# Performance work log

Hardware: AMD Instinct MI355X
Metric: run time of the kernel (lower is better)

## Reference

```python
import jax, jax.numpy as jnp
import numpy as np
from jax.ops import segment_sum

N_NODES = 50000
N_EDGES = 800000
D_IN, D_HID, D_OUT = 128, 128, 64


def setup_inputs() -> dict:
    key = jax.random.key(0)
    ks = jax.random.split(key, 7)
    return {
        "src": jax.random.randint(ks[0], (N_EDGES,), 0, N_NODES, dtype=jnp.int32),
        "dst": jax.random.randint(ks[1], (N_EDGES,), 0, N_NODES, dtype=jnp.int32),
        "x": jax.random.normal(ks[2], (N_NODES, D_IN), dtype=jnp.float32),
        "W1": jax.random.normal(ks[3], (D_IN, D_HID), dtype=jnp.float32) * (1.0 / np.sqrt(D_IN)),
        "b1": jnp.zeros((D_HID,), dtype=jnp.float32),
        "W2": jax.random.normal(ks[4], (D_HID, D_OUT), dtype=jnp.float32) * (1.0 / np.sqrt(D_HID)),
        "b2": jnp.zeros((D_OUT,), dtype=jnp.float32),
    }


def _gcn_layer(src, dst, x, W, b, inv_sqrt_out, inv_sqrt_in):
    # DGL GraphConv, norm='both': h = D_in^{-1/2} A D_out^{-1/2} (x W) + b
    h = (x * inv_sqrt_out[:, None]) @ W          # transform first (in >= out)
    msg = h[src]                                  # gather source messages [E, d]
    agg = segment_sum(msg, dst, num_segments=x.shape[0])
    return agg * inv_sqrt_in[:, None] + b


def reference(src, dst, x, W1, b1, W2, b2):
    n = x.shape[0]
    ones = jnp.ones((src.shape[0],), dtype=x.dtype)
    deg_out = jnp.clip(segment_sum(ones, src, num_segments=n), 1.0)
    deg_in = jnp.clip(segment_sum(ones, dst, num_segments=n), 1.0)
    inv_sqrt_out = jax.lax.rsqrt(deg_out)
    inv_sqrt_in = jax.lax.rsqrt(deg_in)
    h = _gcn_layer(src, dst, x, W1, b1, inv_sqrt_out, inv_sqrt_in)
    h = jax.nn.relu(h)
    h = _gcn_layer(src, dst, h, W2, b2, inv_sqrt_out, inv_sqrt_in)
    return h
```

## Files before the change

### kernel.cpp

```cpp
#include <hip/hip_runtime.h>
#include <hip/hip_fp16.h>

#define D_IN  128
#define D_HID 128
#define D_OUT 64
#define NBMAX 512
#define CHUNK 2048
#define FCACHE 3072

typedef __attribute__((ext_vector_type(8))) short bf16x8;
typedef __attribute__((ext_vector_type(4))) float f32x4;

__device__ __forceinline__ unsigned short f2bf_rne(float f) {
    unsigned int u = __float_as_uint(f);
    return (unsigned short)((u + 0x7FFFu + ((u >> 16) & 1u)) >> 16);
}

__global__ void k_zero(int* __restrict__ cntD, int* __restrict__ cntS, int NB) {
    const int t = threadIdx.x;
    if (t < NB) { cntD[t] = 0; cntS[t] = 0; }
}

__launch_bounds__(256)
__global__ void k_bucket(const int* __restrict__ src, const int* __restrict__ dst,
                         int E, int NB, int cap,
                         int* __restrict__ cntD, int* __restrict__ cntS,
                         unsigned int* __restrict__ storeD, unsigned char* __restrict__ storeS) {
    __shared__ int lcD[NBMAX], lcS[NBMAX];
    __shared__ int lbD[NBMAX], lbS[NBMAX];
    const int t = threadIdx.x;
    const int e0 = blockIdx.x * CHUNK;
    const int e1 = min(e0 + CHUNK, E);

    for (int i = t; i < NB; i += 256) { lcD[i] = 0; lcS[i] = 0; }
    __syncthreads();
    for (int i = e0 + t; i < e1; i += 256) {
        atomicAdd(&lcD[dst[i] >> 7], 1);
        atomicAdd(&lcS[src[i] >> 7], 1);
    }
    __syncthreads();
    for (int i = t; i < NB; i += 256) {
        lbD[i] = lcD[i] ? atomicAdd(&cntD[i], lcD[i]) : 0;
        lbS[i] = lcS[i] ? atomicAdd(&cntS[i], lcS[i]) : 0;
        lcD[i] = 0; lcS[i] = 0;
    }
    __syncthreads();
    for (int i = e0 + t; i < e1; i += 256) {
        const int s = src[i], d = dst[i];
        const int bd = d >> 7;
        const int pd = lbD[bd] + atomicAdd(&lcD[bd], 1);
        storeD[(long long)bd * cap + pd] = (unsigned int)s | ((unsigned int)(d & 127) << 16);
        const int bs = s >> 7;
        const int ps = lbS[bs] + atomicAdd(&lcS[bs], 1);
        storeS[(long long)bs * cap + ps] = (unsigned char)(s & 127);
    }
}

__launch_bounds__(256)
__global__ void k_fin(const unsigned int* __restrict__ storeD, const unsigned char* __restrict__ storeS,
                      const int* __restrict__ cntD, const int* __restrict__ cntS,
                      int cap, int N, int NB, int E,
                      int* __restrict__ rowptr, float* __restrict__ inv_in,
                      float* __restrict__ inv_out, unsigned short* __restrict__ csr_src) {
    __shared__ int fh[128];
    __shared__ int sc[128];
    __shared__ int cur[128];
    __shared__ int red[256];
    __shared__ unsigned int ecache[FCACHE];
    const int b = blockIdx.x, t = threadIdx.x;
    const long long sb = (long long)b * cap;

    int partial = 0;
    for (int i = t; i < b; i += 256) partial += cntD[i];
    red[t] = partial;
    __syncthreads();
    for (int off = 128; off > 0; off >>= 1) {
        if (t < off) red[t] += red[t + off];
        __syncthreads();
    }
    const int base = red[0];

    const int cnt = cntD[b];
    const bool cached = (cnt <= FCACHE);
    if (cached) {
        for (int i = t; i < cnt; i += 256) ecache[i] = storeD[sb + i];
    }

    if (t < 128) fh[t] = 0;
    __syncthreads();
    for (int i = t; i < cnt; i += 256) {
        const unsigned int e = cached ? ecache[i] : storeD[sb + i];
        atomicAdd(&fh[e >> 16], 1);
    }
    __syncthreads();
    if (t < 128) sc[t] = fh[t];
    __syncthreads();
    int inc = (t < 128) ? sc[t] : 0;
    for (int off = 1; off < 128; off <<= 1) {
        int o = (t >= off && t < 128) ? sc[t - off] : 0;
        __syncthreads();
        if (t < 128) { inc += o; sc[t] = inc; }
        __syncthreads();
    }
    if (t < 128) {
        const int excl = inc - fh[t];
        cur[t] = excl;
        const int node = (b << 7) + t;
        if (node < N) {
            rowptr[node] = base + excl;
            inv_in[node] = rsqrtf((float)max(fh[t], 1));
        }
    }
    if (b == NB - 1 && t == 128) rowptr[N] = E;
    __syncthreads();
    for (int i = t; i < cnt; i += 256) {
        const unsigned int e = cached ? ecache[i] : storeD[sb + i];
        const int pos = atomicAdd(&cur[e >> 16], 1);
        csr_src[base + pos] = (unsigned short)(e & 0xFFFFu);
    }

    __syncthreads();
    if (t < 128) fh[t] = 0;
    __syncthreads();
    const int cnts = cntS[b];
    for (int i = t; i < cnts; i += 256) atomicAdd(&fh[storeS[sb + i]], 1);
    __syncthreads();
    if (t < 128) {
        const int node = (b << 7) + t;
        if (node < N) inv_out[node] = rsqrtf((float)max(fh[t], 1));
    }
}

template<int LDN, typename TA>
__launch_bounds__(256)
__global__ void k_gemm_mfma(const TA* __restrict__ X, const float* __restrict__ W,
                            const float* __restrict__ scale, __half* __restrict__ Y, int N) {
    __shared__ short Ah[32][136], Al[32][136];
    __shared__ short Bh[64][136], Bl[64][136];

    const int t = threadIdx.x;
    const int row0 = blockIdx.x * 32;
    const int col0 = blockIdx.y * 64;

    if constexpr (sizeof(TA) == 4) {
#pragma unroll
        for (int p = 0; p < 4; ++p) {
            const int idx = p * 256 + t;
            const int r   = idx >> 5;
            const int c4  = (idx & 31) << 2;
            const int gr  = row0 + r;
            float4 v = make_float4(0.f, 0.f, 0.f, 0.f);
            if (gr < N) {
                v = *(const float4*)((const float*)X + (long long)gr * 128 + c4);
                if (scale) { const float s = scale[gr]; v.x *= s; v.y *= s; v.z *= s; v.w *= s; }
            }
            const float f[4] = {v.x, v.y, v.z, v.w};
            short4 h, l;
            short hh[4], ll[4];
#pragma unroll
            for (int i = 0; i < 4; ++i) {
                const unsigned short hb = f2bf_rne(f[i]);
                const float hf = __uint_as_float(((unsigned int)hb) << 16);
                hh[i] = (short)hb;
                ll[i] = (short)f2bf_rne(f[i] - hf);
            }
            h = make_short4(hh[0], hh[1], hh[2], hh[3]);
            l = make_short4(ll[0], ll[1], ll[2], ll[3]);
            *(short4*)&Ah[r][c4] = h;
            *(short4*)&Al[r][c4] = l;
        }
    } else {
#pragma unroll
        for (int p = 0; p < 2; ++p) {
            const int idx = p * 256 + t;
            const int r   = idx >> 4;
            const int c8  = (idx & 15) << 3;
            const int gr  = row0 + r;
            uint4 raw = make_uint4(0u, 0u, 0u, 0u);
            if (gr < N) raw = *(const uint4*)((const __half*)X + (long long)gr * 128 + c8);
            const __half2* hp = (const __half2*)&raw;
            short hh[8], ll[8];
#pragma unroll
            for (int u = 0; u < 4; ++u) {
                const float2 f2 = __half22float2(hp[u]);
                const float f[2] = {f2.x, f2.y};
#pragma unroll
                for (int q = 0; q < 2; ++q) {
                    const unsigned short hb = f2bf_rne(f[q]);
                    const float hf = __uint_as_float(((unsigned int)hb) << 16);
                    hh[2 * u + q] = (short)hb;
                    ll[2 * u + q] = (short)f2bf_rne(f[q] - hf);
                }
            }
            *(short4*)&Ah[r][c8]     = make_short4(hh[0], hh[1], hh[2], hh[3]);
            *(short4*)&Ah[r][c8 + 4] = make_short4(hh[4], hh[5], hh[6], hh[7]);
            *(short4*)&Al[r][c8]     = make_short4(ll[0], ll[1], ll[2], ll[3]);
            *(short4*)&Al[r][c8 + 4] = make_short4(ll[4], ll[5], ll[6], ll[7]);
        }
    }

#pragma unroll
    for (int p = 0; p < 8; ++p) {
        const int idx = p * 256 + t;
        const int k   = idx >> 4;
        const int c4  = (idx & 15) << 2;
        const float4 v = *(const float4*)(W + (long long)k * LDN + col0 + c4);
        const float f[4] = {v.x, v.y, v.z, v.w};
#pragma unroll
        for (int i = 0; i < 4; ++i) {
            const unsigned short hb = f2bf_rne(f[i]);
            const float hf = __uint_as_float(((unsigned int)hb) << 16);
            Bh[c4 + i][k] = (short)hb;
            Bl[c4 + i][k] = (short)f2bf_rne(f[i] - hf);
        }
    }
    __syncthreads();

    const int w    = t >> 6;
    const int lane = t & 63;
    const int wr = w >> 1, wc = w & 1;
    const int lrow = lane & 15;
    const int lk   = (lane >> 4) << 3;

    f32x4 acc0 = {0.f, 0.f, 0.f, 0.f};
    f32x4 acc1 = {0.f, 0.f, 0.f, 0.f};
#pragma unroll
    for (int ks = 0; ks < 4; ++ks) {
        const int k = ks * 32 + lk;
        const bf16x8 ah  = *(const bf16x8*)&Ah[wr * 16 + lrow][k];
        const bf16x8 al  = *(const bf16x8*)&Al[wr * 16 + lrow][k];
        const bf16x8 bh0 = *(const bf16x8*)&Bh[wc * 32 + lrow][k];
        const bf16x8 bl0 = *(const bf16x8*)&Bl[wc * 32 + lrow][k];
        const bf16x8 bh1 = *(const bf16x8*)&Bh[wc * 32 + 16 + lrow][k];
        const bf16x8 bl1 = *(const bf16x8*)&Bl[wc * 32 + 16 + lrow][k];
        acc0 = __builtin_amdgcn_mfma_f32_16x16x32_bf16(ah, bh0, acc0, 0, 0, 0);
        acc0 = __builtin_amdgcn_mfma_f32_16x16x32_bf16(ah, bl0, acc0, 0, 0, 0);
        acc0 = __builtin_amdgcn_mfma_f32_16x16x32_bf16(al, bh0, acc0, 0, 0, 0);
        acc1 = __builtin_amdgcn_mfma_f32_16x16x32_bf16(ah, bh1, acc1, 0, 0, 0);
        acc1 = __builtin_amdgcn_mfma_f32_16x16x32_bf16(ah, bl1, acc1, 0, 0, 0);
        acc1 = __builtin_amdgcn_mfma_f32_16x16x32_bf16(al, bh1, acc1, 0, 0, 0);
    }

#pragma unroll
    for (int i = 0; i < 4; ++i) {
        const int r = row0 + wr * 16 + ((lane >> 4) << 2) + i;
        if (r < N) {
            Y[(long long)r * LDN + col0 + wc * 32 + lrow]      = __float2half(acc0[i]);
            Y[(long long)r * LDN + col0 + wc * 32 + 16 + lrow] = __float2half(acc1[i]);
        }
    }
}

template<int D, bool RELU, typename TO>
__launch_bounds__(256)
__global__ void k_gather(const int* __restrict__ rowptr, const unsigned short* __restrict__ csr_src,
                         const __half* __restrict__ Y, const float* __restrict__ inv_in,
                         const float* __restrict__ inv_out, const float* __restrict__ b,
                         TO* __restrict__ out, int N) {
    const int wid  = (int)((blockIdx.x * 256u + threadIdx.x) >> 6);
    const int lane = threadIdx.x & 63;
    if (wid >= N) return;

    const int start = rowptr[wid];
    const int end   = rowptr[wid + 1];

    constexpr int LPE = D / 8;
    constexpr int EPW = 64 / LPE;
    const int grp  = lane / LPE;
    const int colh = (lane % LPE) * 8;

    float a[8];
#pragma unroll
    for (int u = 0; u < 8; ++u) a[u] = 0.0f;

    auto accum = [&](uint4 raw) {
        const __half2* h = (const __half2*)&raw;
#pragma unroll
        for (int u = 0; u < 4; ++u) {
            const float2 f = __half22float2(h[u]);
            a[2 * u]     += f.x;
            a[2 * u + 1] += f.y;
        }
    };

    for (int k = start; k < end; k += 64) {
        const int idx = k + lane;
        const int sv  = (idx < end) ? (int)csr_src[idx] : 0;
        const int cnt = min(64, end - k);
        int j = 0;
        for (; j + 4 * EPW <= cnt; j += 4 * EPW) {
            const int s0 = __shfl(sv, j + grp);
            const int s1 = __shfl(sv, j + EPW + grp);
            const int s2 = __shfl(sv, j + 2 * EPW + grp);
            const int s3 = __shfl(sv, j + 3 * EPW + grp);
            const uint4 r0 = *(const uint4*)(Y + (long long)s0 * D + colh);
            const uint4 r1 = *(const uint4*)(Y + (long long)s1 * D + colh);
            const uint4 r2 = *(const uint4*)(Y + (long long)s2 * D + colh);
            const uint4 r3 = *(const uint4*)(Y + (long long)s3 * D + colh);
            accum(r0); accum(r1); accum(r2); accum(r3);
        }
        for (; j < cnt; j += EPW) {
            const int jj = j + grp;
            const int s  = __shfl(sv, jj);
            if (jj < cnt) {
                const uint4 r = *(const uint4*)(Y + (long long)s * D + colh);
                accum(r);
            }
        }
    }

#pragma unroll
    for (int u = 0; u < 8; ++u) a[u] += __shfl_down(a[u], 32);
#pragma unroll
    for (int u = 0; u < 8; ++u) a[u] += __shfl_down(a[u], 16);
    if (EPW == 8) {
#pragma unroll
        for (int u = 0; u < 8; ++u) a[u] += __shfl_down(a[u], 8);
    }

    if (lane < LPE) {
        const float ii = inv_in[wid];
        const float io = RELU ? inv_out[wid] : 0.0f;
        const float4 b0 = *(const float4*)(b + colh);
        const float4 b1 = *(const float4*)(b + colh + 4);
        float r[8];
        r[0] = a[0] * ii + b0.x; r[1] = a[1] * ii + b0.y;
        r[2] = a[2] * ii + b0.z; r[3] = a[3] * ii + b0.w;
        r[4] = a[4] * ii + b1.x; r[5] = a[5] * ii + b1.y;
        r[6] = a[6] * ii + b1.z; r[7] = a[7] * ii + b1.w;
        if (RELU) {
#pragma unroll
            for (int u = 0; u < 8; ++u) r[u] = fmaxf(r[u], 0.0f) * io;
        }
        if constexpr (sizeof(TO) == 2) {
            __half2 h0 = __float22half2_rn(make_float2(r[0], r[1]));
            __half2 h1 = __float22half2_rn(make_float2(r[2], r[3]));
            __half2 h2 = __float22half2_rn(make_float2(r[4], r[5]));
            __half2 h3 = __float22half2_rn(make_float2(r[6], r[7]));
            uint4 pk;
            pk.x = *(unsigned int*)&h0; pk.y = *(unsigned int*)&h1;
            pk.z = *(unsigned int*)&h2; pk.w = *(unsigned int*)&h3;
            *(uint4*)((__half*)out + (long long)wid * D + colh) = pk;
        } else {
            float* o = (float*)out + (long long)wid * D + colh;
            *(float4*)(o)     = make_float4(r[0], r[1], r[2], r[3]);
            *(float4*)(o + 4) = make_float4(r[4], r[5], r[6], r[7]);
        }
    }
}

extern "C" void kernel_launch(void* const* d_in, const int* in_sizes, int n_in,
                              void* d_out, int out_size, void* d_ws, size_t ws_size,
                              hipStream_t stream) {
    const int*   src = (const int*)d_in[0];
    const int*   dst = (const int*)d_in[1];
    const float* x   = (const float*)d_in[2];
    const float* W1  = (const float*)d_in[3];
    const float* b1  = (const float*)d_in[4];
    const float* W2  = (const float*)d_in[5];
    const float* b2  = (const float*)d_in[6];
    float* out = (float*)d_out;

    const int E  = in_sizes[0];
    const int N  = in_sizes[2] / D_IN;
    const int NB = (N + 127) >> 7;
    const int mean = E / NB;
    const int cap  = mean + mean / 4 + 128;

    char* ws = (char*)d_ws;
    size_t off = 0;
    auto alloc = [&](size_t bytes) -> void* {
        void* p = ws + off;
        off += (bytes + 255) & ~(size_t)255;
        return p;
    };
    float*          inv_out = (float*)alloc((size_t)N * 4);
    float*          inv_in  = (float*)alloc((size_t)N * 4);
    int*            rowptr  = (int*)alloc((size_t)(N + 1) * 4);
    int*            cntD    = (int*)alloc((size_t)NB * 4);
    int*            cntS    = (int*)alloc((size_t)NB * 4);
    unsigned int*   storeD  = (unsigned int*)alloc((size_t)NB * cap * 4);
    unsigned char*  storeS  = (unsigned char*)alloc((size_t)NB * cap);
    unsigned short* csr_src = (unsigned short*)alloc((size_t)E * 2);
    __half*         Y1      = (__half*)alloc((size_t)N * D_HID * 2);
    __half*         H       = (__half*)alloc((size_t)N * D_HID * 2);
    __half*         Y2      = (__half*)alloc((size_t)N * D_OUT * 2);
    (void)ws_size; (void)n_in; (void)out_size;

    k_zero<<<1, 512, 0, stream>>>(cntD, cntS, NB);
    k_bucket<<<(E + CHUNK - 1) / CHUNK, 256, 0, stream>>>(src, dst, E, NB, cap, cntD, cntS, storeD, storeS);
    k_fin<<<NB, 256, 0, stream>>>(storeD, storeS, cntD, cntS, cap, N, NB, E,
                                  rowptr, inv_in, inv_out, csr_src);

    {
        dim3 g((N + 31) / 32, D_HID / 64);
        k_gemm_mfma<D_HID, float><<<g, 256, 0, stream>>>(x, W1, inv_out, Y1, N);
    }
    k_gather<D_HID, true, __half><<<(N + 3) / 4, 256, 0, stream>>>(rowptr, csr_src, Y1, inv_in, inv_out, b1, H, N);

    {
        dim3 g((N + 31) / 32, D_OUT / 64);
        k_gemm_mfma<D_OUT, __half><<<g, 256, 0, stream>>>(H, W2, nullptr, Y2, N);
    }
    k_gather<D_OUT, false, float><<<(N + 3) / 4, 256, 0, stream>>>(rowptr, csr_src, Y2, inv_in, nullptr, b2, out, N);
}
```

Baseline: 144.9 us.

## Precompute split-bf16 transposed weights once and read them from global in GEMM

A prep kernel now converts W1 and W2 to transposed hi/lo bf16 pairs once, and it also zeroes the bucket counters. The GEMM no longer converts weights per block into shared memory; each wave reads B fragments straight from global (cache) and one block covers all output columns. This removes the redundant per-block weight conversion and shared-memory staging, and halves the block count for layer 1. The edge bucketing kernel also keeps src/dst in registers so each edge is loaded once instead of twice. The risk is that uncoalesced global B-fragment loads in the MFMA loop add latency compared with shared-memory reads.

```diff
diff --git a/kernel.cpp b/kernel.cpp
--- a/kernel.cpp
+++ b/kernel.cpp
@@ -16,9 +16,31 @@
     return (unsigned short)((u + 0x7FFFu + ((u >> 16) & 1u)) >> 16);
 }
 
-__global__ void k_zero(int* __restrict__ cntD, int* __restrict__ cntS, int NB) {
-    const int t = threadIdx.x;
-    if (t < NB) { cntD[t] = 0; cntS[t] = 0; }
+__launch_bounds__(256)
+__global__ void k_prep(const float* __restrict__ W1, const float* __restrict__ W2,
+                       unsigned short* __restrict__ W1h, unsigned short* __restrict__ W1l,
+                       unsigned short* __restrict__ W2h, unsigned short* __restrict__ W2l,
+                       int* __restrict__ cntD, int* __restrict__ cntS, int NB) {
+    const int b = blockIdx.x, t = threadIdx.x;
+    if (b < 64) {
+        const int i = b * 256 + t;
+        const int k = i >> 7, j = i & 127;
+        const float v = W1[i];
+        const unsigned short hb = f2bf_rne(v);
+        const float hf = __uint_as_float((unsigned int)hb << 16);
+        W1h[j * 128 + k] = hb;
+        W1l[j * 128 + k] = f2bf_rne(v - hf);
+    } else if (b < 96) {
+        const int i = (b - 64) * 256 + t;
+        const int k = i >> 6, j = i & 63;
+        const float v = W2[i];
+        const unsigned short hb = f2bf_rne(v);
+        const float hf = __uint_as_float((unsigned int)hb << 16);
+        W2h[j * 128 + k] = hb;
+        W2l[j * 128 + k] = f2bf_rne(v - hf);
+    } else {
+        for (int i = t; i < NB; i += 256) { cntD[i] = 0; cntS[i] = 0; }
+    }
 }
 
 __launch_bounds__(256)
@@ -32,11 +54,22 @@
     const int e0 = blockIdx.x * CHUNK;
     const int e1 = min(e0 + CHUNK, E);
 
+    int sv[8], dv[8];
+#pragma unroll
+    for (int u = 0; u < 8; ++u) {
+        const int i = e0 + u * 256 + t;
+        if (i < e1) { sv[u] = src[i]; dv[u] = dst[i]; }
+        else        { sv[u] = -1;     dv[u] = -1; }
+    }
+
     for (int i = t; i < NB; i += 256) { lcD[i] = 0; lcS[i] = 0; }
     __syncthreads();
-    for (int i = e0 + t; i < e1; i += 256) {
-        atomicAdd(&lcD[dst[i] >> 7], 1);
-        atomicAdd(&lcS[src[i] >> 7], 1);
+#pragma unroll
+    for (int u = 0; u < 8; ++u) {
+        if (sv[u] >= 0) {
+            atomicAdd(&lcD[dv[u] >> 7], 1);
+            atomicAdd(&lcS[sv[u] >> 7], 1);
+        }
     }
     __syncthreads();
     for (int i = t; i < NB; i += 256) {
@@ -45,14 +78,17 @@
         lcD[i] = 0; lcS[i] = 0;
     }
     __syncthreads();
-    for (int i = e0 + t; i < e1; i += 256) {
-        const int s = src[i], d = dst[i];
-        const int bd = d >> 7;
-        const int pd = lbD[bd] + atomicAdd(&lcD[bd], 1);
-        storeD[(long long)bd * cap + pd] = (unsigned int)s | ((unsigned int)(d & 127) << 16);
-        const int bs = s >> 7;
-        const int ps = lbS[bs] + atomicAdd(&lcS[bs], 1);
-        storeS[(long long)bs * cap + ps] = (unsigned char)(s & 127);
+#pragma unroll
+    for (int u = 0; u < 8; ++u) {
+        if (sv[u] >= 0) {
+            const int s = sv[u], d = dv[u];
+            const int bd = d >> 7;
+            const int pd = lbD[bd] + atomicAdd(&lcD[bd], 1);
+            storeD[(long long)bd * cap + pd] = (unsigned int)s | ((unsigned int)(d & 127) << 16);
+            const int bs = s >> 7;
+            const int ps = lbS[bs] + atomicAdd(&lcS[bs], 1);
+            storeS[(long long)bs * cap + ps] = (unsigned char)(s & 127);
+        }
     }
 }
 
@@ -133,14 +169,14 @@
 
 template<int LDN, typename TA>
 __launch_bounds__(256)
-__global__ void k_gemm_mfma(const TA* __restrict__ X, const float* __restrict__ W,
+__global__ void k_gemm_mfma(const TA* __restrict__ X,
+                            const unsigned short* __restrict__ Wth,
+                            const unsigned short* __restrict__ Wtl,
                             const float* __restrict__ scale, __half* __restrict__ Y, int N) {
     __shared__ short Ah[32][136], Al[32][136];
-    __shared__ short Bh[64][136], Bl[64][136];
 
     const int t = threadIdx.x;
     const int row0 = blockIdx.x * 32;
-    const int col0 = blockIdx.y * 64;
 
     if constexpr (sizeof(TA) == 4) {
 #pragma unroll
@@ -155,7 +191,6 @@
                 if (scale) { const float s = scale[gr]; v.x *= s; v.y *= s; v.z *= s; v.w *= s; }
             }
             const float f[4] = {v.x, v.y, v.z, v.w};
-            short4 h, l;
             short hh[4], ll[4];
 #pragma unroll
             for (int i = 0; i < 4; ++i) {
@@ -164,10 +199,8 @@
                 hh[i] = (short)hb;
                 ll[i] = (short)f2bf_rne(f[i] - hf);
             }
-            h = make_short4(hh[0], hh[1], hh[2], hh[3]);
-            l = make_short4(ll[0], ll[1], ll[2], ll[3]);
-            *(short4*)&Ah[r][c4] = h;
-            *(short4*)&Al[r][c4] = l;
+            *(short4*)&Ah[r][c4] = make_short4(hh[0], hh[1], hh[2], hh[3]);
+            *(short4*)&Al[r][c4] = make_short4(ll[0], ll[1], ll[2], ll[3]);
         }
     } else {
 #pragma unroll
@@ -198,55 +231,43 @@
             *(short4*)&Al[r][c8 + 4] = make_short4(ll[4], ll[5], ll[6], ll[7]);
         }
     }
-
-#pragma unroll
-    for (int p = 0; p < 8; ++p) {
-        const int idx = p * 256 + t;
-        const int k   = idx >> 4;
-        const int c4  = (idx & 15) << 2;
-        const float4 v = *(const float4*)(W + (long long)k * LDN + col0 + c4);
-        const float f[4] = {v.x, v.y, v.z, v.w};
-#pragma unroll
-        for (int i = 0; i < 4; ++i) {
-            const unsigned short hb = f2bf_rne(f[i]);
-            const float hf = __uint_as_float(((unsigned int)hb) << 16);
-            Bh[c4 + i][k] = (short)hb;
-            Bl[c4 + i][k] = (short)f2bf_rne(f[i] - hf);
-        }
-    }
-    __syncthreads();
-
+    __syncthreads();
+
+    constexpr int NT = LDN / 32;
     const int w    = t >> 6;
     const int lane = t & 63;
-    const int wr = w >> 1, wc = w & 1;
+    const int rg = w & 1, cg = w >> 1;
     const int lrow = lane & 15;
     const int lk   = (lane >> 4) << 3;
-
-    f32x4 acc0 = {0.f, 0.f, 0.f, 0.f};
-    f32x4 acc1 = {0.f, 0.f, 0.f, 0.f};
+    const int colbase = cg * (16 * NT);
+
+    f32x4 acc[NT];
+#pragma unroll
+    for (int n = 0; n < NT; ++n) acc[n] = (f32x4){0.f, 0.f, 0.f, 0.f};
+
 #pragma unroll
     for (int ks = 0; ks < 4; ++ks) {
         const int k = ks * 32 + lk;
-        const bf16x8 ah  = *(const bf16x8*)&Ah[wr * 16 + lrow][k];
-        const bf16x8 al  = *(const bf16x8*)&Al[wr * 16 + lrow][k];
-        const bf16x8 bh0 = *(const bf16x8*)&Bh[wc * 32 + lrow][k];
-        const bf16x8 bl0 = *(const bf16x8*)&Bl[wc * 32 + lrow][k];
-        const bf16x8 bh1 = *(const bf16x8*)&Bh[wc * 32 + 16 + lrow][k];
-        const bf16x8 bl1 = *(const bf16x8*)&Bl[wc * 32 + 16 + lrow][k];
-        acc0 = __builtin_amdgcn_mfma_f32_16x16x32_bf16(ah, bh0, acc0, 0, 0, 0);
-        acc0 = __builtin_amdgcn_mfma_f32_16x16x32_bf16(ah, bl0, acc0, 0, 0, 0);
-        acc0 = __builtin_amdgcn_mfma_f32_16x16x32_bf16(al, bh0, acc0, 0, 0, 0);
-        acc1 = __builtin_amdgcn_mfma_f32_16x16x32_bf16(ah, bh1, acc1, 0, 0, 0);
-        acc1 = __builtin_amdgcn_mfma_f32_16x16x32_bf16(ah, bl1, acc1, 0, 0, 0);
-        acc1 = __builtin_amdgcn_mfma_f32_16x16x32_bf16(al, bh1, acc1, 0, 0, 0);
-    }
-
-#pragma unroll
-    for (int i = 0; i < 4; ++i) {
-        const int r = row0 + wr * 16 + ((lane >> 4) << 2) + i;
-        if (r < N) {
-            Y[(long long)r * LDN + col0 + wc * 32 + lrow]      = __float2half(acc0[i]);
-            Y[(long long)r * LDN + col0 + wc * 32 + 16 + lrow] = __float2half(acc1[i]);
+        const bf16x8 ah = *(const bf16x8*)&Ah[rg * 16 + lrow][k];
+        const bf16x8 al = *(const bf16x8*)&Al[rg * 16 + lrow][k];
+#pragma unroll
+        for (int n = 0; n < NT; ++n) {
+            const int col = colbase + n * 16 + lrow;
+            const bf16x8 bh = *(const bf16x8*)(Wth + (size_t)col * 128 + k);
+            const bf16x8 bl = *(const bf16x8*)(Wtl + (size_t)col * 128 + k);
+            acc[n] = __builtin_amdgcn_mfma_f32_16x16x32_bf16(ah, bh, acc[n], 0, 0, 0);
+            acc[n] = __builtin_amdgcn_mfma_f32_16x16x32_bf16(ah, bl, acc[n], 0, 0, 0);
+            acc[n] = __builtin_amdgcn_mfma_f32_16x16x32_bf16(al, bh, acc[n], 0, 0, 0);
+        }
+    }
+
+#pragma unroll
+    for (int n = 0; n < NT; ++n) {
+#pragma unroll
+        for (int i = 0; i < 4; ++i) {
+            const int r = row0 + rg * 16 + ((lane >> 4) << 2) + i;
+            if (r < N)
+                Y[(long long)r * LDN + colbase + n * 16 + lrow] = __float2half(acc[n][i]);
         }
     }
 }
@@ -382,25 +403,23 @@
     unsigned int*   storeD  = (unsigned int*)alloc((size_t)NB * cap * 4);
     unsigned char*  storeS  = (unsigned char*)alloc((size_t)NB * cap);
     unsigned short* csr_src = (unsigned short*)alloc((size_t)E * 2);
+    unsigned short* W1h     = (unsigned short*)alloc(128 * 128 * 2);
+    unsigned short* W1l     = (unsigned short*)alloc(128 * 128 * 2);
+    unsigned short* W2h     = (unsigned short*)alloc(64 * 128 * 2);
+    unsigned short* W2l     = (unsigned short*)alloc(64 * 128 * 2);
     __half*         Y1      = (__half*)alloc((size_t)N * D_HID * 2);
     __half*         H       = (__half*)alloc((size_t)N * D_HID * 2);
     __half*         Y2      = (__half*)alloc((size_t)N * D_OUT * 2);
     (void)ws_size; (void)n_in; (void)out_size;
 
-    k_zero<<<1, 512, 0, stream>>>(cntD, cntS, NB);
+    k_prep<<<97, 256, 0, stream>>>(W1, W2, W1h, W1l, W2h, W2l, cntD, cntS, NB);
     k_bucket<<<(E + CHUNK - 1) / CHUNK, 256, 0, stream>>>(src, dst, E, NB, cap, cntD, cntS, storeD, storeS);
     k_fin<<<NB, 256, 0, stream>>>(storeD, storeS, cntD, cntS, cap, N, NB, E,
                                   rowptr, inv_in, inv_out, csr_src);
 
-    {
-        dim3 g((N + 31) / 32, D_HID / 64);
-        k_gemm_mfma<D_HID, float><<<g, 256, 0, stream>>>(x, W1, inv_out, Y1, N);
-    }
+    k_gemm_mfma<D_HID, float><<<(N + 31) / 32, 256, 0, stream>>>(x, W1h, W1l, inv_out, Y1, N);
     k_gather<D_HID, true, __half><<<(N + 3) / 4, 256, 0, stream>>>(rowptr, csr_src, Y1, inv_in, inv_out, b1, H, N);
 
-    {
-        dim3 g((N + 31) / 32, D_OUT / 64);
-        k_gemm_mfma<D_OUT, __half><<<g, 256, 0, stream>>>(H, W2, nullptr, Y2, N);
-    }
+    k_gemm_mfma<D_OUT, __half><<<(N + 31) / 32, 256, 0, stream>>>(H, W2h, W2l, nullptr, Y2, N);
     k_gather<D_OUT, false, float><<<(N + 3) / 4, 256, 0, stream>>>(rowptr, csr_src, Y2, inv_in, nullptr, b2, out, N);
 }
```

After: 142.3 us. About the same (-1.8%).
